# Kernel tuning notes

Measured on AMD Instinct MI355X. Metric: run time of the kernel, lower is better.

Reference implementation:

```python
import jax, jax.numpy as jnp
import numpy as np

N = 131072          # batch_size(64) * cycle_size(2048) total graph nodes
E = 2097152         # N * avg_degree(16) edges


def _gcn_block(x, edge_index, W_self, W_nbr, b):
    """GraphConv-style STGCN spatial block: self-transform + mean-aggregated
    neighbor transform over edge_index (gather -> segment-reduce -> scatter)."""
    src, dst = edge_index[0], edge_index[1]
    msg = jax.ops.segment_sum(x[src], dst, num_segments=N)            # [N, C_in]
    deg = jax.ops.segment_sum(jnp.ones((edge_index.shape[1],), x.dtype), dst,
                              num_segments=N)                          # [N]
    agg = msg / jnp.maximum(deg, 1.0)[:, None]
    return x @ W_self + agg @ W_nbr + b


def setup_inputs() -> dict:
    key = jax.random.key(0)
    ks = jax.random.split(key, 16)

    def lin(k, fan_in, fan_out):
        return jax.random.normal(k, (fan_in, fan_out), jnp.float32) / np.sqrt(fan_in)

    x = jax.random.normal(ks[0], (N, 16), jnp.float32)
    edge_index = jax.random.randint(ks[1], (2, E), 0, N)
    batch = jnp.zeros((N,), jnp.int64) if jax.config.jax_enable_x64 else jnp.zeros((N,), jnp.int32)

    return {
        "x": x,
        "edge_index": edge_index,
        "batch": batch,
        "W_lin": lin(ks[2], 16, 16),
        "b_lin": jnp.zeros((16,), jnp.float32),
        # block3: 16 -> 32
        "Ws3": lin(ks[3], 16, 32), "Wn3": lin(ks[4], 16, 32), "b3": jnp.zeros((32,), jnp.float32),
        # block2: 32 -> 64
        "Ws2": lin(ks[5], 32, 64), "Wn2": lin(ks[6], 32, 64), "b2": jnp.zeros((64,), jnp.float32),
        # block1: 64 -> 128
        "Ws1": lin(ks[7], 64, 128), "Wn1": lin(ks[8], 64, 128), "b1": jnp.zeros((128,), jnp.float32),
    }


def reference(x, edge_index, batch, W_lin, b_lin,
              Ws3, Wn3, b3, Ws2, Wn2, b2, Ws1, Wn1, b1):
    h = x @ W_lin + b_lin                                   # Linear(16,16)
    h = jax.nn.relu(_gcn_block(h, edge_index, Ws3, Wn3, b3))   # 16 -> 32
    h = jax.nn.relu(_gcn_block(h, edge_index, Ws2, Wn2, b2))   # 32 -> 64
    h = jax.nn.sigmoid(_gcn_block(h, edge_index, Ws1, Wn1, b1))  # 64 -> 128
    return h
```

## Files before the change

### kernel.cpp

```cpp
#include <hip/hip_runtime.h>
#include <cmath>


typedef __attribute__((ext_vector_type(8))) _Float16 half8;
typedef __attribute__((ext_vector_type(4))) float floatx4;

#define NBUCKET 512
#define BUCKET_SHIFT 8

__global__ __launch_bounds__(256) void bucket_hist_kernel(
    const int* __restrict__ dst, int* __restrict__ bcnt, int E, int EPB, int nblk) {
    __shared__ int lh[NBUCKET];
    for (int i = threadIdx.x; i < NBUCKET; i += 256) lh[i] = 0;
    __syncthreads();
    int base = blockIdx.x * EPB;
    int end  = min(base + EPB, E);
    for (int i = base + threadIdx.x; i < end; i += 256)
        atomicAdd(&lh[dst[i] >> BUCKET_SHIFT], 1);
    __syncthreads();
    for (int i = threadIdx.x; i < NBUCKET; i += 256)
        bcnt[i * nblk + blockIdx.x] = lh[i];
}

__global__ void scan1_kernel(const int* __restrict__ in, int* __restrict__ out,
                             int* __restrict__ bsum) {
    __shared__ int s[256];
    int i = blockIdx.x * 256 + threadIdx.x;
    int v = in[i];
    s[threadIdx.x] = v;
    __syncthreads();
    for (int off = 1; off < 256; off <<= 1) {
        int t = (threadIdx.x >= off) ? s[threadIdx.x - off] : 0;
        __syncthreads();
        s[threadIdx.x] += t;
        __syncthreads();
    }
    out[i] = s[threadIdx.x] - v;
    if (threadIdx.x == 255) bsum[blockIdx.x] = s[255];
}

__global__ void scan2_kernel(int* __restrict__ bsum, int NB) {
    extern __shared__ int s2[];
    int v = (threadIdx.x < NB) ? bsum[threadIdx.x] : 0;
    s2[threadIdx.x] = v;
    __syncthreads();
    for (int off = 1; off < NB; off <<= 1) {
        int t = (threadIdx.x >= off) ? s2[threadIdx.x - off] : 0;
        __syncthreads();
        s2[threadIdx.x] += t;
        __syncthreads();
    }
    if (threadIdx.x < NB) bsum[threadIdx.x] = s2[threadIdx.x] - v;
}

__global__ void scan3_kernel(int* __restrict__ out, const int* __restrict__ bsum) {
    int i = blockIdx.x * 256 + threadIdx.x;
    out[i] += bsum[blockIdx.x];
}

__global__ __launch_bounds__(256) void partition_kernel(
    const int* __restrict__ src, const int* __restrict__ dst,
    const int* __restrict__ bofs, int2* __restrict__ part,
    int E, int EPB, int nblk) {
    __shared__ int cur[NBUCKET];
    for (int i = threadIdx.x; i < NBUCKET; i += 256)
        cur[i] = bofs[i * nblk + blockIdx.x];
    __syncthreads();
    int base = blockIdx.x * EPB;
    int end  = min(base + EPB, E);
    for (int i = base + threadIdx.x; i < end; i += 256) {
        int d = dst[i];
        int p = atomicAdd(&cur[d >> BUCKET_SHIFT], 1);
        part[p] = make_int2(src[i], d);
    }
}

__global__ __launch_bounds__(256) void local_csr_kernel(
    const int* __restrict__ bofs, const int2* __restrict__ part,
    int* __restrict__ row_ptr, int* __restrict__ csr_src,
    int N, int E, int nblk) {
    __shared__ int cnt[256];
    __shared__ int offs[256];
    const int u      = blockIdx.x;
    const int node0  = u << BUCKET_SHIFT;
    const int bstart = bofs[(size_t)u * nblk];
    const int bend   = (u + 1 < gridDim.x) ? bofs[(size_t)(u + 1) * nblk] : E;

    cnt[threadIdx.x] = 0;
    __syncthreads();
    for (int i = bstart + threadIdx.x; i < bend; i += 256)
        atomicAdd(&cnt[part[i].y - node0], 1);
    __syncthreads();

    int v = cnt[threadIdx.x];
    offs[threadIdx.x] = v;
    __syncthreads();
    for (int off = 1; off < 256; off <<= 1) {
        int t = (threadIdx.x >= off) ? offs[threadIdx.x - off] : 0;
        __syncthreads();
        offs[threadIdx.x] += t;
        __syncthreads();
    }
    int excl = offs[threadIdx.x] - v;
    int rbase = bstart + excl;
    if (node0 + threadIdx.x < N) row_ptr[node0 + threadIdx.x] = rbase;
    if (u == 0 && threadIdx.x == 0) row_ptr[N] = E;
    __syncthreads();
    cnt[threadIdx.x] = rbase;
    __syncthreads();
    for (int i = bstart + threadIdx.x; i < bend; i += 256) {
        int2 e = part[i];
        int p = atomicAdd(&cnt[e.y - node0], 1);
        csr_src[p] = e.x;
    }
}

__global__ void wt_kernel(const float* __restrict__ Ws, const float* __restrict__ Wn,
                          _Float16* __restrict__ Wt, int CI, int NOUT) {
    int K = 2 * CI;
    int idx = blockIdx.x * 256 + threadIdx.x;
    if (idx >= NOUT * K) return;
    int n = idx / K, k = idx - n * K;
    float v = (k < CI) ? Ws[(size_t)k * NOUT + n] : Wn[(size_t)(k - CI) * NOUT + n];
    Wt[idx] = (_Float16)v;
}

__global__ void lin16_kernel(const float* __restrict__ x, const float* __restrict__ W,
                             const float* __restrict__ b, _Float16* __restrict__ h, int N) {
    __shared__ float sW[256];
    __shared__ float sb[16];
    sW[threadIdx.x] = W[threadIdx.x];
    if (threadIdx.x < 16) sb[threadIdx.x] = b[threadIdx.x];
    __syncthreads();
    int n = blockIdx.x * blockDim.x + threadIdx.x;
    if (n >= N) return;
    const float4* xr = (const float4*)(x + (size_t)n * 16);
    float4 x0 = xr[0], x1 = xr[1], x2 = xr[2], x3 = xr[3];
    float xi[16] = {x0.x, x0.y, x0.z, x0.w, x1.x, x1.y, x1.z, x1.w,
                    x2.x, x2.y, x2.z, x2.w, x3.x, x3.y, x3.z, x3.w};
    float o[16];
#pragma unroll
    for (int j = 0; j < 16; j++) o[j] = sb[j];
#pragma unroll
    for (int k = 0; k < 16; k++) {
        float xv = xi[k];
#pragma unroll
        for (int j = 0; j < 16; j++) o[j] += xv * sW[k * 16 + j];
    }
    half8 h0v, h1v;
#pragma unroll
    for (int j = 0; j < 8; j++) { h0v[j] = (_Float16)o[j]; h1v[j] = (_Float16)o[j + 8]; }
    half8* hr = (half8*)(h + (size_t)n * 16);
    hr[0] = h0v;
    hr[1] = h1v;
}

template <int C>
__global__ void gather_kernel(const int* __restrict__ row_ptr, const int* __restrict__ csr_src,
                              const _Float16* __restrict__ h, _Float16* __restrict__ agg, int N) {
    constexpr int GP = C / 8;
    int t = blockIdx.x * blockDim.x + threadIdx.x;
    int total = N * GP;
    if (t >= total) return;
    int n = t / GP;
    int g = t - n * GP;
    const int beg = row_ptr[n];
    const int end = row_ptr[n + 1];
    const size_t goff = (size_t)g * 8;

    float a0[8], a1[8];
#pragma unroll
    for (int i = 0; i < 8; i++) { a0[i] = 0.f; a1[i] = 0.f; }

    int j = beg;
    for (; j + 4 <= end; j += 4) {
        int i0 = csr_src[j + 0], i1 = csr_src[j + 1], i2 = csr_src[j + 2], i3 = csr_src[j + 3];
        half8 v0 = *(const half8*)(h + (size_t)i0 * C + goff);
        half8 v1 = *(const half8*)(h + (size_t)i1 * C + goff);
        half8 v2 = *(const half8*)(h + (size_t)i2 * C + goff);
        half8 v3 = *(const half8*)(h + (size_t)i3 * C + goff);
#pragma unroll
        for (int i = 0; i < 8; i++) {
            a0[i] += (float)v0[i] + (float)v2[i];
            a1[i] += (float)v1[i] + (float)v3[i];
        }
    }
    for (; j < end; ++j) {
        int i0 = csr_src[j];
        half8 v0 = *(const half8*)(h + (size_t)i0 * C + goff);
#pragma unroll
        for (int i = 0; i < 8; i++) a0[i] += (float)v0[i];
    }

    float inv = 1.0f / fmaxf((float)(end - beg), 1.0f);
    half8 r;
#pragma unroll
    for (int i = 0; i < 8; i++) r[i] = (_Float16)((a0[i] + a1[i]) * inv);
    *(half8*)(agg + (size_t)n * C + goff) = r;
}

template <int CI, int NOUT, int ACT, bool OUT_F16>
__global__ __launch_bounds__(256) void mfma_gemm_kernel(
    const _Float16* __restrict__ hbuf, const _Float16* __restrict__ abuf,
    const _Float16* __restrict__ Wt,
    const float* __restrict__ bias, void* __restrict__ outp, int N)
{
    constexpr int K   = 2 * CI;
    constexpr int KS  = K / 32;
    constexpr int CT  = NOUT / 16;
    constexpr int LDW = K + 8;
    __shared__ _Float16 Bt[NOUT * LDW];

    const int tid = threadIdx.x;
    for (int idx = tid; idx < NOUT * (K / 8); idx += 256) {
        int n  = idx / (K / 8);
        int kq = idx - n * (K / 8);
        *(half8*)&Bt[n * LDW + kq * 8] = *(const half8*)(Wt + (size_t)n * K + kq * 8);
    }
    __syncthreads();

    const int wave = tid >> 6;
    const int lane = tid & 63;
    const int m    = lane & 15;
    const int quad = lane >> 4;
    const int row0 = blockIdx.x * 64 + wave * 16;
    const size_t row = (size_t)(row0 + m);

    floatx4 acc[CT];
#pragma unroll
    for (int c = 0; c < CT; c++) acc[c] = (floatx4){0.f, 0.f, 0.f, 0.f};

#pragma unroll
    for (int s = 0; s < KS; s++) {
        int k8 = s * 32 + quad * 8;
        const _Float16* Ap = (k8 < CI) ? (hbuf + row * CI + k8)
                                       : (abuf + row * CI + (k8 - CI));
        half8 a = *(const half8*)Ap;
#pragma unroll
        for (int c = 0; c < CT; c++) {
            half8 b = *(const half8*)&Bt[(c * 16 + m) * LDW + k8];
            acc[c] = __builtin_amdgcn_mfma_f32_16x16x32_f16(a, b, acc[c], 0, 0, 0);
        }
    }

#pragma unroll
    for (int c = 0; c < CT; c++) {
        int col = c * 16 + m;
        float bv = bias[col];
#pragma unroll
        for (int j = 0; j < 4; j++) {
            int orow = row0 + quad * 4 + j;
            float v = acc[c][j] + bv;
            if (ACT == 0) v = fmaxf(v, 0.0f);
            else          v = 1.0f / (1.0f + __expf(-v));
            if (OUT_F16) ((_Float16*)outp)[(size_t)orow * NOUT + col] = (_Float16)v;
            else         ((float*)outp)[(size_t)orow * NOUT + col] = v;
        }
    }
}

extern "C" void kernel_launch(void* const* d_in, const int* in_sizes, int n_in,
                              void* d_out, int out_size, void* d_ws, size_t ws_size,
                              hipStream_t stream) {
    const float* x     = (const float*)d_in[0];
    const int*   ei    = (const int*)d_in[1];
    const float* W_lin = (const float*)d_in[3];
    const float* b_lin = (const float*)d_in[4];
    const float* Ws3   = (const float*)d_in[5];
    const float* Wn3   = (const float*)d_in[6];
    const float* b3    = (const float*)d_in[7];
    const float* Ws2   = (const float*)d_in[8];
    const float* Wn2   = (const float*)d_in[9];
    const float* b2    = (const float*)d_in[10];
    const float* Ws1   = (const float*)d_in[11];
    const float* Wn1   = (const float*)d_in[12];
    const float* b1    = (const float*)d_in[13];
    float* out = (float*)d_out;

    const int N = in_sizes[0] / 16;
    const int E = in_sizes[1] / 2;
    const int* src = ei;
    const int* dst = ei + E;

    const int NBLK = 512;
    const int EPB  = (E + NBLK - 1) / NBLK;
    const int M    = NBUCKET * NBLK;
    const int NB2  = M / 256;

    int* wsi = (int*)d_ws;
    int* row_ptr = wsi;
    size_t B0 = ((size_t)(N + 1) + 3) & ~(size_t)3;
    int* bcnt = wsi + B0;
    int* bofs = bcnt + M;
    int* bsum = bofs + M;
    size_t C0 = (B0 + 2 * (size_t)M + (size_t)NB2 + 3) & ~(size_t)3;
    int* csr_src = wsi + C0;
    size_t P0 = (C0 + (size_t)E + 3) & ~(size_t)3;
    int2* part = (int2*)(wsi + P0);
    size_t H0 = (P0 + 2 * (size_t)E + 3) & ~(size_t)3;
    _Float16* regA = (_Float16*)(wsi + H0);
    _Float16* regB = regA + (size_t)64 * N;
    _Float16* Wt1  = regB + (size_t)64 * N;
    _Float16* Wt2  = Wt1 + 16384;
    _Float16* Wt3  = Wt2 + 4096;

    _Float16* h0    = regA;
    _Float16* agg16 = regA + (size_t)16 * N;
    _Float16* h2    = regA;
    _Float16* h3    = regB;
    _Float16* agg32 = regB + (size_t)32 * N;
    _Float16* agg64 = regB;

    const int BLK = 256;

    wt_kernel<<<(32 * 32 + 255) / 256, 256, 0, stream>>>(Ws3, Wn3, Wt3, 16, 32);
    wt_kernel<<<(64 * 64 + 255) / 256, 256, 0, stream>>>(Ws2, Wn2, Wt2, 32, 64);
    wt_kernel<<<(128 * 128 + 255) / 256, 256, 0, stream>>>(Ws1, Wn1, Wt1, 64, 128);

    bucket_hist_kernel<<<NBLK, 256, 0, stream>>>(dst, bcnt, E, EPB, NBLK);
    scan1_kernel<<<NB2, 256, 0, stream>>>(bcnt, bofs, bsum);
    scan2_kernel<<<1, NB2, NB2 * sizeof(int), stream>>>(bsum, NB2);
    scan3_kernel<<<NB2, 256, 0, stream>>>(bofs, bsum);
    partition_kernel<<<NBLK, 256, 0, stream>>>(src, dst, bofs, part, E, EPB, NBLK);
    local_csr_kernel<<<NBUCKET, 256, 0, stream>>>(bofs, part, row_ptr, csr_src, N, E, NBLK);

    lin16_kernel<<<(N + BLK - 1) / BLK, BLK, 0, stream>>>(x, W_lin, b_lin, h0, N);

    gather_kernel<16><<<((size_t)N * 2 + BLK - 1) / BLK, BLK, 0, stream>>>(row_ptr, csr_src, h0, agg16, N);
    mfma_gemm_kernel<16, 32, 0, true><<<N / 64, 256, 0, stream>>>(h0, agg16, Wt3, b3, h3, N);

    gather_kernel<32><<<((size_t)N * 4 + BLK - 1) / BLK, BLK, 0, stream>>>(row_ptr, csr_src, h3, agg32, N);
    mfma_gemm_kernel<32, 64, 0, true><<<N / 64, 256, 0, stream>>>(h3, agg32, Wt2, b2, h2, N);

    gather_kernel<64><<<((size_t)N * 8 + BLK - 1) / BLK, BLK, 0, stream>>>(row_ptr, csr_src, h2, agg64, N);
    mfma_gemm_kernel<64, 128, 1, false><<<N / 64, 256, 0, stream>>>(h2, agg64, Wt1, b1, out, N);
}
```

Baseline: 339.4 us.

## Sort CSR neighbors by source range and widen gather to 16 channels per thread

The local CSR build now sub-buckets each destination's edges into 8 ranges by source node id, so neighbor lists come out roughly sorted by source, which should make gathered rows more cache-local. The gather kernel processes 16 channels per thread instead of 8, halving the thread count and index reloads, and replaces the scalar tail loop with a masked 4-wide step. Index loads and output stores use nontemporal hints. Costs are 8x more shared-memory counters in the CSR kernel, more registers per gather thread and less parallelism.

```diff
diff --git a/kernel.cpp b/kernel.cpp
--- a/kernel.cpp
+++ b/kernel.cpp
@@ -78,39 +78,45 @@
 __global__ __launch_bounds__(256) void local_csr_kernel(
     const int* __restrict__ bofs, const int2* __restrict__ part,
     int* __restrict__ row_ptr, int* __restrict__ csr_src,
-    int N, int E, int nblk) {
-    __shared__ int cnt[256];
-    __shared__ int offs[256];
+    int N, int E, int nblk, int sh) {
+    __shared__ int cnt2[256 * 8];
+    __shared__ int s[256];
     const int u      = blockIdx.x;
     const int node0  = u << BUCKET_SHIFT;
     const int bstart = bofs[(size_t)u * nblk];
     const int bend   = (u + 1 < gridDim.x) ? bofs[(size_t)(u + 1) * nblk] : E;
-
-    cnt[threadIdx.x] = 0;
-    __syncthreads();
-    for (int i = bstart + threadIdx.x; i < bend; i += 256)
-        atomicAdd(&cnt[part[i].y - node0], 1);
-    __syncthreads();
-
-    int v = cnt[threadIdx.x];
-    offs[threadIdx.x] = v;
+    const int tid = threadIdx.x;
+
+    for (int k = tid; k < 256 * 8; k += 256) cnt2[k] = 0;
+    __syncthreads();
+    for (int i = bstart + tid; i < bend; i += 256) {
+        int2 e = part[i];
+        atomicAdd(&cnt2[((e.y - node0) << 3) + (e.x >> sh)], 1);
+    }
+    __syncthreads();
+
+    int loc[8];
+    int tot = 0;
+#pragma unroll
+    for (int k = 0; k < 8; k++) { loc[k] = tot; tot += cnt2[tid * 8 + k]; }
+    s[tid] = tot;
     __syncthreads();
     for (int off = 1; off < 256; off <<= 1) {
-        int t = (threadIdx.x >= off) ? offs[threadIdx.x - off] : 0;
-        __syncthreads();
-        offs[threadIdx.x] += t;
-        __syncthreads();
-    }
-    int excl = offs[threadIdx.x] - v;
+        int t2 = (tid >= off) ? s[tid - off] : 0;
+        __syncthreads();
+        s[tid] += t2;
+        __syncthreads();
+    }
+    int excl  = s[tid] - tot;
     int rbase = bstart + excl;
-    if (node0 + threadIdx.x < N) row_ptr[node0 + threadIdx.x] = rbase;
-    if (u == 0 && threadIdx.x == 0) row_ptr[N] = E;
-    __syncthreads();
-    cnt[threadIdx.x] = rbase;
-    __syncthreads();
-    for (int i = bstart + threadIdx.x; i < bend; i += 256) {
+    if (node0 + tid < N) row_ptr[node0 + tid] = rbase;
+    if (u == 0 && tid == 0) row_ptr[N] = E;
+#pragma unroll
+    for (int k = 0; k < 8; k++) cnt2[tid * 8 + k] = rbase + loc[k];
+    __syncthreads();
+    for (int i = bstart + tid; i < bend; i += 256) {
         int2 e = part[i];
-        int p = atomicAdd(&cnt[e.y - node0], 1);
+        int p = atomicAdd(&cnt2[((e.y - node0) << 3) + (e.x >> sh)], 1);
         csr_src[p] = e.x;
     }
 }
@@ -156,47 +162,73 @@
 }
 
 template <int C>
-__global__ void gather_kernel(const int* __restrict__ row_ptr, const int* __restrict__ csr_src,
-                              const _Float16* __restrict__ h, _Float16* __restrict__ agg, int N) {
-    constexpr int GP = C / 8;
-    int t = blockIdx.x * blockDim.x + threadIdx.x;
-    int total = N * GP;
-    if (t >= total) return;
+__global__ __launch_bounds__(256) void gather_kernel(
+    const int* __restrict__ row_ptr, const int* __restrict__ csr_src,
+    const _Float16* __restrict__ h, _Float16* __restrict__ agg, int N) {
+    constexpr int GP = C / 16;
+    int t = blockIdx.x * 256 + threadIdx.x;
+    if (t >= N * GP) return;
     int n = t / GP;
     int g = t - n * GP;
     const int beg = row_ptr[n];
     const int end = row_ptr[n + 1];
-    const size_t goff = (size_t)g * 8;
-
-    float a0[8], a1[8];
-#pragma unroll
-    for (int i = 0; i < 8; i++) { a0[i] = 0.f; a1[i] = 0.f; }
+    const size_t goff = (size_t)g * 16;
+
+    float a[16];
+#pragma unroll
+    for (int i = 0; i < 16; i++) a[i] = 0.f;
 
     int j = beg;
     for (; j + 4 <= end; j += 4) {
-        int i0 = csr_src[j + 0], i1 = csr_src[j + 1], i2 = csr_src[j + 2], i3 = csr_src[j + 3];
-        half8 v0 = *(const half8*)(h + (size_t)i0 * C + goff);
-        half8 v1 = *(const half8*)(h + (size_t)i1 * C + goff);
-        half8 v2 = *(const half8*)(h + (size_t)i2 * C + goff);
-        half8 v3 = *(const half8*)(h + (size_t)i3 * C + goff);
+        int i0 = __builtin_nontemporal_load(csr_src + j + 0);
+        int i1 = __builtin_nontemporal_load(csr_src + j + 1);
+        int i2 = __builtin_nontemporal_load(csr_src + j + 2);
+        int i3 = __builtin_nontemporal_load(csr_src + j + 3);
+        const half8* r0 = (const half8*)(h + (size_t)i0 * C + goff);
+        const half8* r1 = (const half8*)(h + (size_t)i1 * C + goff);
+        const half8* r2 = (const half8*)(h + (size_t)i2 * C + goff);
+        const half8* r3 = (const half8*)(h + (size_t)i3 * C + goff);
+        half8 v0l = r0[0], v0h = r0[1];
+        half8 v1l = r1[0], v1h = r1[1];
+        half8 v2l = r2[0], v2h = r2[1];
+        half8 v3l = r3[0], v3h = r3[1];
 #pragma unroll
         for (int i = 0; i < 8; i++) {
-            a0[i] += (float)v0[i] + (float)v2[i];
-            a1[i] += (float)v1[i] + (float)v3[i];
+            a[i]     += ((float)v0l[i] + (float)v1l[i]) + ((float)v2l[i] + (float)v3l[i]);
+            a[i + 8] += ((float)v0h[i] + (float)v1h[i]) + ((float)v2h[i] + (float)v3h[i]);
         }
     }
-    for (; j < end; ++j) {
+    if (j < end) {
+        const int last = end - 1;
         int i0 = csr_src[j];
-        half8 v0 = *(const half8*)(h + (size_t)i0 * C + goff);
-#pragma unroll
-        for (int i = 0; i < 8; i++) a0[i] += (float)v0[i];
+        int i1 = csr_src[min(j + 1, last)];
+        int i2 = csr_src[min(j + 2, last)];
+        int i3 = csr_src[min(j + 3, last)];
+        const half8* r0 = (const half8*)(h + (size_t)i0 * C + goff);
+        const half8* r1 = (const half8*)(h + (size_t)i1 * C + goff);
+        const half8* r2 = (const half8*)(h + (size_t)i2 * C + goff);
+        const half8* r3 = (const half8*)(h + (size_t)i3 * C + goff);
+        half8 v0l = r0[0], v0h = r0[1];
+        half8 v1l = r1[0], v1h = r1[1];
+        half8 v2l = r2[0], v2h = r2[1];
+        half8 v3l = r3[0], v3h = r3[1];
+        float w1 = (j + 1 < end) ? 1.f : 0.f;
+        float w2 = (j + 2 < end) ? 1.f : 0.f;
+        float w3 = (j + 3 < end) ? 1.f : 0.f;
+#pragma unroll
+        for (int i = 0; i < 8; i++) {
+            a[i]     += ((float)v0l[i] + w1 * (float)v1l[i]) + (w2 * (float)v2l[i] + w3 * (float)v3l[i]);
+            a[i + 8] += ((float)v0h[i] + w1 * (float)v1h[i]) + (w2 * (float)v2h[i] + w3 * (float)v3h[i]);
+        }
     }
 
     float inv = 1.0f / fmaxf((float)(end - beg), 1.0f);
-    half8 r;
-#pragma unroll
-    for (int i = 0; i < 8; i++) r[i] = (_Float16)((a0[i] + a1[i]) * inv);
-    *(half8*)(agg + (size_t)n * C + goff) = r;
+    half8 rl, rh;
+#pragma unroll
+    for (int i = 0; i < 8; i++) { rl[i] = (_Float16)(a[i] * inv); rh[i] = (_Float16)(a[i + 8] * inv); }
+    half8* ap = (half8*)(agg + (size_t)n * C + goff);
+    __builtin_nontemporal_store(rl, ap);
+    __builtin_nontemporal_store(rh, ap + 1);
 }
 
 template <int CI, int NOUT, int ACT, bool OUT_F16>
@@ -286,6 +318,8 @@
     const int EPB  = (E + NBLK - 1) / NBLK;
     const int M    = NBUCKET * NBLK;
     const int NB2  = M / 256;
+    int LOGN = 0; while ((1 << (LOGN + 1)) <= N) LOGN++;
+    const int SH = (LOGN >= 3) ? (LOGN - 3) : 0;
 
     int* wsi = (int*)d_ws;
     int* row_ptr = wsi;
@@ -322,16 +356,16 @@
     scan2_kernel<<<1, NB2, NB2 * sizeof(int), stream>>>(bsum, NB2);
     scan3_kernel<<<NB2, 256, 0, stream>>>(bofs, bsum);
     partition_kernel<<<NBLK, 256, 0, stream>>>(src, dst, bofs, part, E, EPB, NBLK);
-    local_csr_kernel<<<NBUCKET, 256, 0, stream>>>(bofs, part, row_ptr, csr_src, N, E, NBLK);
+    local_csr_kernel<<<NBUCKET, 256, 0, stream>>>(bofs, part, row_ptr, csr_src, N, E, NBLK, SH);
 
     lin16_kernel<<<(N + BLK - 1) / BLK, BLK, 0, stream>>>(x, W_lin, b_lin, h0, N);
 
-    gather_kernel<16><<<((size_t)N * 2 + BLK - 1) / BLK, BLK, 0, stream>>>(row_ptr, csr_src, h0, agg16, N);
+    gather_kernel<16><<<((size_t)N * 1 + BLK - 1) / BLK, BLK, 0, stream>>>(row_ptr, csr_src, h0, agg16, N);
     mfma_gemm_kernel<16, 32, 0, true><<<N / 64, 256, 0, stream>>>(h0, agg16, Wt3, b3, h3, N);
 
-    gather_kernel<32><<<((size_t)N * 4 + BLK - 1) / BLK, BLK, 0, stream>>>(row_ptr, csr_src, h3, agg32, N);
+    gather_kernel<32><<<((size_t)N * 2 + BLK - 1) / BLK, BLK, 0, stream>>>(row_ptr, csr_src, h3, agg32, N);
     mfma_gemm_kernel<32, 64, 0, true><<<N / 64, 256, 0, stream>>>(h3, agg32, Wt2, b2, h2, N);
 
-    gather_kernel<64><<<((size_t)N * 8 + BLK - 1) / BLK, BLK, 0, stream>>>(row_ptr, csr_src, h2, agg64, N);
+    gather_kernel<64><<<((size_t)N * 4 + BLK - 1) / BLK, BLK, 0, stream>>>(row_ptr, csr_src, h2, agg64, N);
     mfma_gemm_kernel<64, 128, 1, false><<<N / 64, 256, 0, stream>>>(h2, agg64, Wt1, b1, out, N);
 }
```

Measured after the change: 342.9 us. No clear change (+1.0%).
